# Performance work log

Hardware: AMD Instinct MI355X
Metric: run time of the kernel (lower is better)

The kernel has to match this reference:

```python
import jax, jax.numpy as jnp
import numpy as np

N = 100000
E = 1600000
D_IN = 256
D_OUT = 128
ALPHA = 0.2  # LeakyReLU negative slope


def setup_inputs() -> dict:
    key = jax.random.key(0)
    k1, k2, k3, k4, k5 = jax.random.split(key, 5)
    x = jax.random.normal(k1, (N, D_IN), dtype=jnp.float32)
    # random edges + self-loops so every destination row has >=1 incoming edge
    src = jax.random.randint(k2, (E - N,), 0, N)
    dst = jax.random.randint(k3, (E - N,), 0, N)
    loops = jnp.arange(N)
    edge = jnp.stack([jnp.concatenate([src, loops]),
                      jnp.concatenate([dst, loops])]).astype(jnp.int64)  # [2, E]
    W = jax.random.normal(k4, (D_IN, D_OUT), dtype=jnp.float32) * 0.1
    a = jax.random.normal(k5, (1, 2 * D_OUT), dtype=jnp.float32) * 0.1
    return {"x": x, "edge": edge, "W": W, "a": a}


def reference(x, edge, W, a):
    n = x.shape[0]
    d_out = W.shape[1]
    h = x @ W  # [n, d_out]
    src, dst = edge[0], edge[1]
    # a @ concat(h[src], h[dst]) decomposes into two per-node projections
    f_src = h @ a[0, :d_out]   # [n]
    f_dst = h @ a[0, d_out:]   # [n]
    tmp = f_src[src] + f_dst[dst]                      # [E]
    lrelu = jnp.where(tmp > 0, tmp, ALPHA * tmp)
    edge_e = jnp.exp(-lrelu)                           # [E]
    # spmm(A, ones) -> rowsum; spmm(A, h) -> weighted aggregation (rows = src)
    e_rowsum = jax.ops.segment_sum(edge_e, src, num_segments=n)           # [n]
    hh = jax.ops.segment_sum(edge_e[:, None] * h[dst], src, num_segments=n)  # [n, d_out]
    hh = hh / e_rowsum[:, None]
    return jax.nn.elu(hh)  # end=False -> apply ELU
```

## Files before the change

kernel.cpp:

```cpp
#include <hip/hip_runtime.h>

#define D_IN 256
#define D_OUT 128
#define ALPHA 0.2f
#define RB 64
#define RBSH 6
#define NBMAX 1600
#define CH 8192
#define CAPG 1536
#define OVFCAP 32768
#define LKH 128

typedef __attribute__((ext_vector_type(8))) short bf16x8;
typedef __attribute__((ext_vector_type(4))) float f32x4;

__device__ inline unsigned short f2bf(float f) {
    unsigned int u = __float_as_uint(f);
    return (unsigned short)((u + 0x7FFFu + ((u >> 16) & 1u)) >> 16);
}
__device__ inline float bf2f(unsigned short u) {
    return __uint_as_float(((unsigned int)u) << 16);
}
__device__ inline unsigned int cvt_pk_bf16(float lo, float hi) {
    unsigned int r;
    asm("v_cvt_pk_bf16_f32 %0, %1, %2" : "=v"(r) : "v"(lo), "v"(hi));
    return r;
}

__global__ __launch_bounds__(256) void k_wt(const float* __restrict__ W,
                                            unsigned short* __restrict__ WTb) {
    const int ncol = blockIdx.x;
    const int k = threadIdx.x;
    WTb[(size_t)ncol * 256 + k] = f2bf(W[(size_t)k * 128 + ncol]);
}

__global__ __launch_bounds__(256) void k_gemm(const float* __restrict__ x,
                                              const unsigned short* __restrict__ WTb,
                                              const float* __restrict__ a,
                                              unsigned short* __restrict__ hb,
                                              float* __restrict__ f_src,
                                              float* __restrict__ f_dst, int n) {
    __shared__ unsigned short sA[128 * LKH];
    __shared__ float sFp[128][2][2];
    const int t = threadIdx.x;
    const int l = t & 63;
    const int w = t >> 6;
    const int wr = w >> 1, wc = w & 1;
    const int row0 = blockIdx.x * 128;
    const int col0 = wc * 64;
    const int lr = l & 15;
    const int g = l >> 4;
    const int lk8 = g * 8;

    f32x4 acc[4][4] = {};
    const unsigned short* bp[4];
    #pragma unroll
    for (int ni = 0; ni < 4; ++ni)
        bp[ni] = WTb + (size_t)(col0 + ni * 16 + lr) * 256 + lk8;

    #pragma unroll
    for (int half = 0; half < 2; ++half) {
        {
            const int rr = t >> 4;
            const int cc = (t & 15) * 8;
            #pragma unroll
            for (int it = 0; it < 8; ++it) {
                int r = it * 16 + rr;
                int gr = row0 + r;
                float4 fa, fb;
                if (gr < n) {
                    const float* xp = &x[(size_t)gr * D_IN + half * LKH + cc];
                    fa = *(const float4*)xp;
                    fb = *(const float4*)(xp + 4);
                } else {
                    fa = make_float4(0.f, 0.f, 0.f, 0.f);
                    fb = fa;
                }
                uint4 v;
                v.x = cvt_pk_bf16(fa.x, fa.y);
                v.y = cvt_pk_bf16(fa.z, fa.w);
                v.z = cvt_pk_bf16(fb.x, fb.y);
                v.w = cvt_pk_bf16(fb.z, fb.w);
                int js = (cc >> 3) ^ ((r & 7) << 1);
                *(uint4*)&sA[r * LKH + js * 8] = v;
            }
        }
        __syncthreads();

        #pragma unroll
        for (int k0 = 0; k0 < LKH; k0 += 32) {
            bf16x8 af[4], bfr[4];
            #pragma unroll
            for (int mi = 0; mi < 4; ++mi) {
                int row_l = wr * 64 + mi * 16 + lr;
                int js = ((k0 >> 3) + g) ^ ((row_l & 7) << 1);
                af[mi] = *(const bf16x8*)&sA[row_l * LKH + js * 8];
            }
            #pragma unroll
            for (int ni = 0; ni < 4; ++ni)
                bfr[ni] = *(const bf16x8*)(bp[ni] + half * LKH + k0);
            #pragma unroll
            for (int mi = 0; mi < 4; ++mi)
                #pragma unroll
                for (int ni = 0; ni < 4; ++ni)
                    acc[mi][ni] = __builtin_amdgcn_mfma_f32_16x16x32_bf16(
                        af[mi], bfr[ni], acc[mi][ni], 0, 0, 0);
        }
        __syncthreads();
    }

    #pragma unroll
    for (int mi = 0; mi < 4; ++mi) {
        #pragma unroll
        for (int q = 0; q < 4; ++q) {
            int r = row0 + wr * 64 + mi * 16 + g * 4 + q;
            if (r < n) {
                unsigned int a01 = cvt_pk_bf16(acc[mi][0][q], acc[mi][1][q]);
                unsigned int a23 = cvt_pk_bf16(acc[mi][2][q], acc[mi][3][q]);
                unsigned short* hp = &hb[(size_t)r * D_OUT + col0 + lr];
                hp[0]  = (unsigned short)(a01 & 0xFFFF);
                hp[16] = (unsigned short)(a01 >> 16);
                hp[32] = (unsigned short)(a23 & 0xFFFF);
                hp[48] = (unsigned short)(a23 >> 16);
            }
        }
    }

    float asv[4], adv[4];
    #pragma unroll
    for (int ni = 0; ni < 4; ++ni) {
        asv[ni] = a[col0 + ni * 16 + lr];
        adv[ni] = a[D_OUT + col0 + ni * 16 + lr];
    }
    #pragma unroll
    for (int mi = 0; mi < 4; ++mi) {
        #pragma unroll
        for (int q = 0; q < 4; ++q) {
            float fs = 0.f, fd = 0.f;
            #pragma unroll
            for (int ni = 0; ni < 4; ++ni) {
                float v = acc[mi][ni][q];
                fs = fmaf(v, asv[ni], fs);
                fd = fmaf(v, adv[ni], fd);
            }
            #pragma unroll
            for (int m = 1; m < 16; m <<= 1) {
                fs += __shfl_xor(fs, m);
                fd += __shfl_xor(fd, m);
            }
            if (lr == 0) {
                int rl = wr * 64 + mi * 16 + g * 4 + q;
                sFp[rl][wc][0] = fs;
                sFp[rl][wc][1] = fd;
            }
        }
    }
    __syncthreads();
    if (t < 128) {
        int r = row0 + t;
        if (r < n) {
            f_src[r] = sFp[t][0][0] + sFp[t][1][0];
            f_dst[r] = sFp[t][0][1] + sFp[t][1][1];
        }
    }
}

__global__ __launch_bounds__(256) void k_bfill(const int* __restrict__ src,
                                               const int* __restrict__ dst,
                                               int* __restrict__ gcnt,
                                               int2* __restrict__ ovf,
                                               int* __restrict__ gkeys, int E, int nb) {
    __shared__ int cnt[NBMAX];
    __shared__ int bas[NBMAX];
    const int t = threadIdx.x;
    const int e0 = blockIdx.x * CH;
    const int e1 = min(e0 + CH, E);
    for (int i = t; i < nb; i += 256) cnt[i] = 0;
    __syncthreads();
    for (int e = e0 + t; e < e1; e += 256) atomicAdd(&cnt[src[e] >> RBSH], 1);
    __syncthreads();
    for (int b = t; b < nb; b += 256) {
        int c = cnt[b];
        bas[b] = c ? atomicAdd(&gcnt[b], c) : 0;
        cnt[b] = 0;
    }
    __syncthreads();
    for (int e = e0 + t; e < e1; e += 256) {
        int s = src[e], d = dst[e];
        int b = s >> RBSH;
        int key = ((s & (RB - 1)) << 17) | d;
        int r = bas[b] + atomicAdd(&cnt[b], 1);
        if (r < CAPG) {
            gkeys[b * CAPG + r] = key;
        } else {
            int o = atomicAdd(&gcnt[nb], 1);
            if (o < OVFCAP) ovf[o] = make_int2(b, key);
        }
    }
}

__global__ __launch_bounds__(512, 8) void k_bagg(const unsigned short* __restrict__ hb,
                                                 const float* __restrict__ f_src,
                                                 const float* __restrict__ f_dst,
                                                 const int* __restrict__ gcnt,
                                                 const int2* __restrict__ ovf,
                                                 const int* __restrict__ gkeys,
                                                 float* __restrict__ out, int n, int nb) {
    __shared__ int2 sdw[CAPG];
    __shared__ int nbase[RB];
    __shared__ int ncnt[RB];
    __shared__ int ncur[RB];
    __shared__ float fsl[RB];
    __shared__ int sc[RB];
    const int t = threadIdx.x;
    const int b = blockIdx.x;
    const int s0 = b * RB;
    const int nn = min(RB, n - s0);
    const int beg = b * CAPG;
    const int stored = min(gcnt[b], CAPG);
    const int ovf_n = min(gcnt[nb], OVFCAP);

    for (int i = t; i < RB; i += 512) {
        ncnt[i] = 0;
        fsl[i] = (i < nn) ? f_src[s0 + i] : 0.f;
    }
    __syncthreads();

    for (int i = t; i < stored; i += 512)
        atomicAdd(&ncnt[gkeys[beg + i] >> 17], 1);
    __syncthreads();

    if (t < RB) sc[t] = ncnt[t];
    __syncthreads();
    for (int off = 1; off < RB; off <<= 1) {
        int v = 0;
        if (t < RB && t >= off) v = sc[t - off];
        __syncthreads();
        if (t < RB) sc[t] += v;
        __syncthreads();
    }
    if (t < RB) {
        nbase[t] = sc[t] - ncnt[t];
        ncur[t]  = sc[t] - ncnt[t];
    }
    __syncthreads();

    for (int i = t; i < stored; i += 512) {
        int k = gkeys[beg + i];
        int d = k & 0x1FFFF, ls = k >> 17;
        float tmp = fsl[ls] + f_dst[d];
        float w = __expf(-((tmp > 0.f) ? tmp : ALPHA * tmp));
        int pos = atomicAdd(&ncur[ls], 1);
        sdw[pos] = make_int2(d, __float_as_int(w));
    }
    __syncthreads();

    const int lane = t & 63, wid = t >> 6;
    const int cl = (lane & 31) * 4;
    const bool isB = lane >= 32;
    for (int ni = wid; ni < nn; ni += 8) {
        const int jb = nbase[ni];
        const int cn = ncnt[ni];
        const int halfA = (cn + 1) >> 1;
        const int halfB = cn - halfA;
        const int lim = isB ? halfB : halfA;
        const int jbh = jb + (isB ? halfA : 0);
        float a0 = 0.f, a1 = 0.f, a2 = 0.f, a3 = 0.f, rowsum = 0.f;
        #pragma unroll 4
        for (int it = 0; it < halfA; ++it) {
            bool valid = it < lim;
            int2 dw = sdw[valid ? (jbh + it) : jb];
            float w = valid ? __int_as_float(dw.y) : 0.f;
            ushort4 hv = *(const ushort4*)&hb[(size_t)dw.x * D_OUT + cl];
            rowsum += w;
            a0 = fmaf(w, bf2f(hv.x), a0);
            a1 = fmaf(w, bf2f(hv.y), a1);
            a2 = fmaf(w, bf2f(hv.z), a2);
            a3 = fmaf(w, bf2f(hv.w), a3);
        }
        if (ovf_n > 0) {
            for (int o = 0; o < ovf_n; ++o) {
                int2 ov = ovf[o];
                if (ov.x == b && (ov.y >> 17) == ni && !isB) {
                    int d = ov.y & 0x1FFFF;
                    float tmp = fsl[ni] + f_dst[d];
                    float w = __expf(-((tmp > 0.f) ? tmp : ALPHA * tmp));
                    ushort4 hv = *(const ushort4*)&hb[(size_t)d * D_OUT + cl];
                    rowsum += w;
                    a0 = fmaf(w, bf2f(hv.x), a0);
                    a1 = fmaf(w, bf2f(hv.y), a1);
                    a2 = fmaf(w, bf2f(hv.z), a2);
                    a3 = fmaf(w, bf2f(hv.w), a3);
                }
            }
        }
        rowsum += __shfl_xor(rowsum, 32);
        a0 += __shfl_xor(a0, 32);
        a1 += __shfl_xor(a1, 32);
        a2 += __shfl_xor(a2, 32);
        a3 += __shfl_xor(a3, 32);
        if (!isB) {
            float inv = 1.f / rowsum;
            a0 *= inv; a1 *= inv; a2 *= inv; a3 *= inv;
            a0 = (a0 > 0.f) ? a0 : (__expf(a0) - 1.f);
            a1 = (a1 > 0.f) ? a1 : (__expf(a1) - 1.f);
            a2 = (a2 > 0.f) ? a2 : (__expf(a2) - 1.f);
            a3 = (a3 > 0.f) ? a3 : (__expf(a3) - 1.f);
            *(float4*)&out[(size_t)(s0 + ni) * D_OUT + cl] =
                make_float4(a0, a1, a2, a3);
        }
    }
}

extern "C" void kernel_launch(void* const* d_in, const int* in_sizes, int n_in,
                              void* d_out, int out_size, void* d_ws, size_t ws_size,
                              hipStream_t stream) {
    const float* x    = (const float*)d_in[0];
    const int*   edge = (const int*)d_in[1];
    const float* W    = (const float*)d_in[2];
    const float* a    = (const float*)d_in[3];
    float* out = (float*)d_out;

    const int n = in_sizes[0] / D_IN;
    const int E = in_sizes[1] / 2;
    const int* src = edge;
    const int* dst = edge + E;
    const int nb = (n + RB - 1) / RB;

    char* p = (char*)d_ws;
    unsigned short* hb  = (unsigned short*)p; p += (size_t)n * D_OUT * sizeof(unsigned short);
    unsigned short* WTb = (unsigned short*)p; p += (size_t)D_OUT * D_IN * sizeof(unsigned short);
    float* f_src = (float*)p;  p += (size_t)n * sizeof(float);
    float* f_dst = (float*)p;  p += (size_t)n * sizeof(float);
    int*  gcnt   = (int*)p;    p += (size_t)(nb + 1) * sizeof(int);
    int2* ovf    = (int2*)p;   p += (size_t)OVFCAP * sizeof(int2);
    int*  gkeys  = (int*)p;    p += (size_t)nb * CAPG * sizeof(int);

    const int gemm_blocks = (n + 127) / 128;

    k_wt<<<D_OUT, 256, 0, stream>>>(W, WTb);
    k_gemm<<<gemm_blocks, 256, 0, stream>>>(x, WTb, a, hb, f_src, f_dst, n);

    hipMemsetAsync(gcnt, 0, (size_t)(nb + 1) * sizeof(int), stream);
    k_bfill<<<(E + CH - 1) / CH, 256, 0, stream>>>(src, dst, gcnt, ovf, gkeys, E, nb);
    k_bagg<<<nb, 512, 0, stream>>>(hb, f_src, f_dst, gcnt, ovf, gkeys, out, n, nb);
}
```

Measured before the change: 151.4 us.

## Load GEMM A-operand directly from global into registers; shrink aggregation blocks

The GEMM kernel no longer stages x tiles through shared memory with block-wide barriers. Each lane now loads its float rows straight from global memory, converts them to bf16 in registers and feeds the MFMA, with out-of-range rows clamped to the last row. The aggregation kernel drops from 512 to 256 threads per block, so each wave handles more destination rows. This removes LDS traffic and syncs in the GEMM, but global loads become less coalesced and are not double-buffered, and the aggregation kernel has less parallelism per block.

Result: slower. 165.9 us (+9.6%).

```diff
diff --git a/kernel.cpp b/kernel.cpp
--- a/kernel.cpp
+++ b/kernel.cpp
@@ -9,7 +9,6 @@
 #define CH 8192
 #define CAPG 1536
 #define OVFCAP 32768
-#define LKH 128
 
 typedef __attribute__((ext_vector_type(8))) short bf16x8;
 typedef __attribute__((ext_vector_type(4))) float f32x4;
@@ -40,7 +39,6 @@
                                               unsigned short* __restrict__ hb,
                                               float* __restrict__ f_src,
                                               float* __restrict__ f_dst, int n) {
-    __shared__ unsigned short sA[128 * LKH];
     __shared__ float sFp[128][2][2];
     const int t = threadIdx.x;
     const int l = t & 63;
@@ -53,60 +51,42 @@
     const int lk8 = g * 8;
 
     f32x4 acc[4][4] = {};
+
+    const float* ap[4];
+    #pragma unroll
+    for (int mi = 0; mi < 4; ++mi) {
+        int r = row0 + wr * 64 + mi * 16 + lr;
+        if (r > n - 1) r = n - 1;
+        ap[mi] = x + (size_t)r * D_IN + lk8;
+    }
     const unsigned short* bp[4];
     #pragma unroll
     for (int ni = 0; ni < 4; ++ni)
         bp[ni] = WTb + (size_t)(col0 + ni * 16 + lr) * 256 + lk8;
 
     #pragma unroll
-    for (int half = 0; half < 2; ++half) {
-        {
-            const int rr = t >> 4;
-            const int cc = (t & 15) * 8;
-            #pragma unroll
-            for (int it = 0; it < 8; ++it) {
-                int r = it * 16 + rr;
-                int gr = row0 + r;
-                float4 fa, fb;
-                if (gr < n) {
-                    const float* xp = &x[(size_t)gr * D_IN + half * LKH + cc];
-                    fa = *(const float4*)xp;
-                    fb = *(const float4*)(xp + 4);
-                } else {
-                    fa = make_float4(0.f, 0.f, 0.f, 0.f);
-                    fb = fa;
-                }
-                uint4 v;
-                v.x = cvt_pk_bf16(fa.x, fa.y);
-                v.y = cvt_pk_bf16(fa.z, fa.w);
-                v.z = cvt_pk_bf16(fb.x, fb.y);
-                v.w = cvt_pk_bf16(fb.z, fb.w);
-                int js = (cc >> 3) ^ ((r & 7) << 1);
-                *(uint4*)&sA[r * LKH + js * 8] = v;
-            }
-        }
-        __syncthreads();
-
-        #pragma unroll
-        for (int k0 = 0; k0 < LKH; k0 += 32) {
-            bf16x8 af[4], bfr[4];
-            #pragma unroll
-            for (int mi = 0; mi < 4; ++mi) {
-                int row_l = wr * 64 + mi * 16 + lr;
-                int js = ((k0 >> 3) + g) ^ ((row_l & 7) << 1);
-                af[mi] = *(const bf16x8*)&sA[row_l * LKH + js * 8];
-            }
+    for (int k0 = 0; k0 < D_IN; k0 += 32) {
+        bf16x8 af[4], bfr[4];
+        #pragma unroll
+        for (int mi = 0; mi < 4; ++mi) {
+            float4 fa = *(const float4*)(ap[mi] + k0);
+            float4 fb = *(const float4*)(ap[mi] + k0 + 4);
+            union { uint4 u; bf16x8 v; } cv;
+            cv.u.x = cvt_pk_bf16(fa.x, fa.y);
+            cv.u.y = cvt_pk_bf16(fa.z, fa.w);
+            cv.u.z = cvt_pk_bf16(fb.x, fb.y);
+            cv.u.w = cvt_pk_bf16(fb.z, fb.w);
+            af[mi] = cv.v;
+        }
+        #pragma unroll
+        for (int ni = 0; ni < 4; ++ni)
+            bfr[ni] = *(const bf16x8*)(bp[ni] + k0);
+        #pragma unroll
+        for (int mi = 0; mi < 4; ++mi)
             #pragma unroll
             for (int ni = 0; ni < 4; ++ni)
-                bfr[ni] = *(const bf16x8*)(bp[ni] + half * LKH + k0);
-            #pragma unroll
-            for (int mi = 0; mi < 4; ++mi)
-                #pragma unroll
-                for (int ni = 0; ni < 4; ++ni)
-                    acc[mi][ni] = __builtin_amdgcn_mfma_f32_16x16x32_bf16(
-                        af[mi], bfr[ni], acc[mi][ni], 0, 0, 0);
-        }
-        __syncthreads();
+                acc[mi][ni] = __builtin_amdgcn_mfma_f32_16x16x32_bf16(
+                    af[mi], bfr[ni], acc[mi][ni], 0, 0, 0);
     }
 
     #pragma unroll
@@ -199,7 +179,7 @@
     }
 }
 
-__global__ __launch_bounds__(512, 8) void k_bagg(const unsigned short* __restrict__ hb,
+__global__ __launch_bounds__(256, 8) void k_bagg(const unsigned short* __restrict__ hb,
                                                  const float* __restrict__ f_src,
                                                  const float* __restrict__ f_dst,
                                                  const int* __restrict__ gcnt,
@@ -220,13 +200,13 @@
     const int stored = min(gcnt[b], CAPG);
     const int ovf_n = min(gcnt[nb], OVFCAP);
 
-    for (int i = t; i < RB; i += 512) {
+    for (int i = t; i < RB; i += 256) {
         ncnt[i] = 0;
         fsl[i] = (i < nn) ? f_src[s0 + i] : 0.f;
     }
     __syncthreads();
 
-    for (int i = t; i < stored; i += 512)
+    for (int i = t; i < stored; i += 256)
         atomicAdd(&ncnt[gkeys[beg + i] >> 17], 1);
     __syncthreads();
 
@@ -245,7 +225,7 @@
     }
     __syncthreads();
 
-    for (int i = t; i < stored; i += 512) {
+    for (int i = t; i < stored; i += 256) {
         int k = gkeys[beg + i];
         int d = k & 0x1FFFF, ls = k >> 17;
         float tmp = fsl[ls] + f_dst[d];
@@ -258,7 +238,7 @@
     const int lane = t & 63, wid = t >> 6;
     const int cl = (lane & 31) * 4;
     const bool isB = lane >= 32;
-    for (int ni = wid; ni < nn; ni += 8) {
+    for (int ni = wid; ni < nn; ni += 4) {
         const int jb = nbase[ni];
         const int cn = ncnt[ni];
         const int halfA = (cn + 1) >> 1;
@@ -343,5 +323,5 @@
 
     hipMemsetAsync(gcnt, 0, (size_t)(nb + 1) * sizeof(int), stream);
     k_bfill<<<(E + CH - 1) / CH, 256, 0, stream>>>(src, dst, gcnt, ovf, gkeys, E, nb);
-    k_bagg<<<nb, 512, 0, stream>>>(hb, f_src, f_dst, gcnt, ovf, gkeys, out, n, nb);
-}
+    k_bagg<<<nb, 256, 0, stream>>>(hb, f_src, f_dst, gcnt, ovf, gkeys, out, n, nb);
+}
```

## Merge edge bucketing and GEMM into one launch; shrink GEMM row tile

Applied to the files above, without the earlier changes.

Folds the edge-bucketing kernel into the GEMM kernel as a set of leading blocks, so bucketing and the x@W projection run concurrently in a single launch instead of back to back. The GEMM row tile drops from 128 to 64 to match the shared-memory footprint shared with the bucketing path, which doubles the number of GEMM blocks. The memset of the bucket counters moves before the launches. This removes one launch and a serialization point, but each GEMM block now does less work per W-fragment load, and block scheduling becomes heterogeneous.

Result: faster. 133.5 us (-11.8%).

```diff
diff --git a/kernel.cpp b/kernel.cpp
--- a/kernel.cpp
+++ b/kernel.cpp
@@ -10,6 +10,7 @@
 #define CAPG 1536
 #define OVFCAP 32768
 #define LKH 128
+#define BM 64
 
 typedef __attribute__((ext_vector_type(8))) short bf16x8;
 typedef __attribute__((ext_vector_type(4))) float f32x4;
@@ -34,25 +35,63 @@
     WTb[(size_t)ncol * 256 + k] = f2bf(W[(size_t)k * 128 + ncol]);
 }
 
-__global__ __launch_bounds__(256) void k_gemm(const float* __restrict__ x,
-                                              const unsigned short* __restrict__ WTb,
-                                              const float* __restrict__ a,
-                                              unsigned short* __restrict__ hb,
-                                              float* __restrict__ f_src,
-                                              float* __restrict__ f_dst, int n) {
-    __shared__ unsigned short sA[128 * LKH];
-    __shared__ float sFp[128][2][2];
+__global__ __launch_bounds__(256) void k_fused(const float* __restrict__ x,
+                                               const unsigned short* __restrict__ WTb,
+                                               const float* __restrict__ a,
+                                               unsigned short* __restrict__ hb,
+                                               float* __restrict__ f_src,
+                                               float* __restrict__ f_dst, int n,
+                                               const int* __restrict__ src,
+                                               const int* __restrict__ dst,
+                                               int* __restrict__ gcnt,
+                                               int2* __restrict__ ovf,
+                                               int* __restrict__ gkeys, int E, int nb,
+                                               int nbf) {
+    __shared__ char smem[BM * LKH * 2];
+    __shared__ float sFp[BM][2][2];
     const int t = threadIdx.x;
+
+    if (blockIdx.x < nbf) {
+        int* cnt = (int*)smem;
+        int* bas = cnt + NBMAX;
+        const int e0 = blockIdx.x * CH;
+        const int e1 = min(e0 + CH, E);
+        for (int i = t; i < nb; i += 256) cnt[i] = 0;
+        __syncthreads();
+        for (int e = e0 + t; e < e1; e += 256) atomicAdd(&cnt[src[e] >> RBSH], 1);
+        __syncthreads();
+        for (int b = t; b < nb; b += 256) {
+            int c = cnt[b];
+            bas[b] = c ? atomicAdd(&gcnt[b], c) : 0;
+            cnt[b] = 0;
+        }
+        __syncthreads();
+        for (int e = e0 + t; e < e1; e += 256) {
+            int s = src[e], d = dst[e];
+            int b = s >> RBSH;
+            int key = ((s & (RB - 1)) << 17) | d;
+            int r = bas[b] + atomicAdd(&cnt[b], 1);
+            if (r < CAPG) {
+                gkeys[b * CAPG + r] = key;
+            } else {
+                int o = atomicAdd(&gcnt[nb], 1);
+                if (o < OVFCAP) ovf[o] = make_int2(b, key);
+            }
+        }
+        return;
+    }
+
+    unsigned short* sA = (unsigned short*)smem;
     const int l = t & 63;
     const int w = t >> 6;
     const int wr = w >> 1, wc = w & 1;
-    const int row0 = blockIdx.x * 128;
+    const int row0 = (blockIdx.x - nbf) * BM;
     const int col0 = wc * 64;
     const int lr = l & 15;
     const int g = l >> 4;
     const int lk8 = g * 8;
 
-    f32x4 acc[4][4] = {};
+    f32x4 acc[2][4] = {};
     const unsigned short* bp[4];
     #pragma unroll
     for (int ni = 0; ni < 4; ++ni)
@@ -64,7 +103,7 @@
             const int rr = t >> 4;
             const int cc = (t & 15) * 8;
             #pragma unroll
-            for (int it = 0; it < 8; ++it) {
+            for (int it = 0; it < 4; ++it) {
                 int r = it * 16 + rr;
                 int gr = row0 + r;
                 float4 fa, fb;
@@ -89,10 +128,10 @@
 
         #pragma unroll
         for (int k0 = 0; k0 < LKH; k0 += 32) {
-            bf16x8 af[4], bfr[4];
-            #pragma unroll
-            for (int mi = 0; mi < 4; ++mi) {
-                int row_l = wr * 64 + mi * 16 + lr;
+            bf16x8 af[2], bfr[4];
+            #pragma unroll
+            for (int mi = 0; mi < 2; ++mi) {
+                int row_l = wr * 32 + mi * 16 + lr;
                 int js = ((k0 >> 3) + g) ^ ((row_l & 7) << 1);
                 af[mi] = *(const bf16x8*)&sA[row_l * LKH + js * 8];
             }
@@ -100,7 +139,7 @@
             for (int ni = 0; ni < 4; ++ni)
                 bfr[ni] = *(const bf16x8*)(bp[ni] + half * LKH + k0);
             #pragma unroll
-            for (int mi = 0; mi < 4; ++mi)
+            for (int mi = 0; mi < 2; ++mi)
                 #pragma unroll
                 for (int ni = 0; ni < 4; ++ni)
                     acc[mi][ni] = __builtin_amdgcn_mfma_f32_16x16x32_bf16(
@@ -110,10 +149,10 @@
     }
 
     #pragma unroll
-    for (int mi = 0; mi < 4; ++mi) {
+    for (int mi = 0; mi < 2; ++mi) {
         #pragma unroll
         for (int q = 0; q < 4; ++q) {
-            int r = row0 + wr * 64 + mi * 16 + g * 4 + q;
+            int r = row0 + wr * 32 + mi * 16 + g * 4 + q;
             if (r < n) {
                 unsigned int a01 = cvt_pk_bf16(acc[mi][0][q], acc[mi][1][q]);
                 unsigned int a23 = cvt_pk_bf16(acc[mi][2][q], acc[mi][3][q]);
@@ -133,7 +172,7 @@
         adv[ni] = a[D_OUT + col0 + ni * 16 + lr];
     }
     #pragma unroll
-    for (int mi = 0; mi < 4; ++mi) {
+    for (int mi = 0; mi < 2; ++mi) {
         #pragma unroll
         for (int q = 0; q < 4; ++q) {
             float fs = 0.f, fd = 0.f;
@@ -149,52 +188,18 @@
                 fd += __shfl_xor(fd, m);
             }
             if (lr == 0) {
-                int rl = wr * 64 + mi * 16 + g * 4 + q;
+                int rl = wr * 32 + mi * 16 + g * 4 + q;
                 sFp[rl][wc][0] = fs;
                 sFp[rl][wc][1] = fd;
             }
         }
     }
     __syncthreads();
-    if (t < 128) {
+    if (t < BM) {
         int r = row0 + t;
         if (r < n) {
             f_src[r] = sFp[t][0][0] + sFp[t][1][0];
             f_dst[r] = sFp[t][0][1] + sFp[t][1][1];
-        }
-    }
-}
-
-__global__ __launch_bounds__(256) void k_bfill(const int* __restrict__ src,
-                                               const int* __restrict__ dst,
-                                               int* __restrict__ gcnt,
-                                               int2* __restrict__ ovf,
-                                               int* __restrict__ gkeys, int E, int nb) {
-    __shared__ int cnt[NBMAX];
-    __shared__ int bas[NBMAX];
-    const int t = threadIdx.x;
-    const int e0 = blockIdx.x * CH;
-    const int e1 = min(e0 + CH, E);
-    for (int i = t; i < nb; i += 256) cnt[i] = 0;
-    __syncthreads();
-    for (int e = e0 + t; e < e1; e += 256) atomicAdd(&cnt[src[e] >> RBSH], 1);
-    __syncthreads();
-    for (int b = t; b < nb; b += 256) {
-        int c = cnt[b];
-        bas[b] = c ? atomicAdd(&gcnt[b], c) : 0;
-        cnt[b] = 0;
-    }
-    __syncthreads();
-    for (int e = e0 + t; e < e1; e += 256) {
-        int s = src[e], d = dst[e];
-        int b = s >> RBSH;
-        int key = ((s & (RB - 1)) << 17) | d;
-        int r = bas[b] + atomicAdd(&cnt[b], 1);
-        if (r < CAPG) {
-            gkeys[b * CAPG + r] = key;
-        } else {
-            int o = atomicAdd(&gcnt[nb], 1);
-            if (o < OVFCAP) ovf[o] = make_int2(b, key);
         }
     }
 }
@@ -336,12 +341,12 @@
     int2* ovf    = (int2*)p;   p += (size_t)OVFCAP * sizeof(int2);
     int*  gkeys  = (int*)p;    p += (size_t)nb * CAPG * sizeof(int);
 
-    const int gemm_blocks = (n + 127) / 128;
-
+    const int gemm_blocks = (n + BM - 1) / BM;
+    const int nbf = (E + CH - 1) / CH;
+
+    hipMemsetAsync(gcnt, 0, (size_t)(nb + 1) * sizeof(int), stream);
     k_wt<<<D_OUT, 256, 0, stream>>>(W, WTb);
-    k_gemm<<<gemm_blocks, 256, 0, stream>>>(x, WTb, a, hb, f_src, f_dst, n);
-
-    hipMemsetAsync(gcnt, 0, (size_t)(nb + 1) * sizeof(int), stream);
-    k_bfill<<<(E + CH - 1) / CH, 256, 0, stream>>>(src, dst, gcnt, ovf, gkeys, E, nb);
+    k_fused<<<nbf + gemm_blocks, 256, 0, stream>>>(x, WTb, a, hb, f_src, f_dst, n,
+                                                   src, dst, gcnt, ovf, gkeys, E, nb, nbf);
     k_bagg<<<nb, 512, 0, stream>>>(hb, f_src, f_dst, gcnt, ovf, gkeys, out, n, nb);
 }
```
